# Performance work log

Hardware: AMD Instinct MI355X
Metric: run time of the kernel (lower is better)

## Reference

```python
import jax, jax.numpy as jnp
import numpy as np

D_MODEL, N_STATE, L_MAX, BATCH = 256, 64, 2048, 16

def _to_c(x):
    return jax.lax.complex(x[..., 0], x[..., 1])

def setup_inputs() -> dict:
    key = jax.random.key(0)
    k_u, k_ct_r, k_ct_i, k_step = jax.random.split(key, 4)
    n, d = N_STATE, D_MODEL
    # --- HiPPO DPLR init (numpy, matches torch hippo_dplr) ---
    P = np.sqrt(1.0 + 2.0 * np.arange(1, n + 1, dtype=np.float64))
    A = np.tril(np.outer(P, P)) - np.diag(np.arange(1, n + 1, dtype=np.float64))
    A = -A
    p = 0.5 * np.sqrt(2.0 * np.arange(1, n + 1, dtype=np.float64) + 1.0)
    Ap = (A + np.outer(p, p)).astype(np.complex64)
    lam, V = np.linalg.eig(Ap)
    p_rot = V.conj().T @ p.astype(np.complex64)
    p_ri = np.stack([p_rot.real, p_rot.imag], -1).astype(np.float32)          # (n,2)
    lambda_ri = np.stack([lam.real, lam.imag], -1).astype(np.float32)         # (n,2)
    # --- B init: sqrt(2k+1), repeated over channels, zero imag ---
    B_r = np.sqrt(2.0 * np.arange(1, n + 1) + 1.0).astype(np.float32)
    B_ri = np.stack([np.tile(B_r, (d, 1)), np.zeros((d, n), np.float32)], -1) # (d,n,2)
    # --- Ct: xavier-normal complex ---
    std = float(np.sqrt(2.0 / (d + n)))
    Ct_r = jax.random.normal(k_ct_r, (d, n), jnp.float32) * (std / np.sqrt(2.0))
    Ct_i = jax.random.normal(k_ct_i, (d, n), jnp.float32) * (std / np.sqrt(2.0))
    Ct_ri = jnp.stack([Ct_r, Ct_i], -1)                                        # (d,n,2)
    Dp = jnp.ones((1, 1, d), jnp.float32)
    log_step = jax.random.uniform(k_step, (d,), jnp.float32) * (
        np.log(0.1) - np.log(0.001)) + np.log(0.001)
    u = jax.random.normal(k_u, (BATCH, L_MAX, d), jnp.float32)
    return {"u": u, "p_ri": jnp.asarray(p_ri), "lambda_ri": jnp.asarray(lambda_ri),
            "B_ri": jnp.asarray(B_ri), "Ct_ri": Ct_ri, "Dp": Dp, "log_step": log_step}

def reference(u, p_ri, lambda_ri, B_ri, Ct_ri, Dp, log_step):
    p = _to_c(p_ri)          # (n,)
    lam = _to_c(lambda_ri)   # (n,)
    B = _to_c(B_ri)          # (d,n)
    Ct = _to_c(Ct_ri)        # (d,n)
    L = u.shape[1]
    omega = jnp.exp(2j * jnp.pi * jnp.arange(L) / L).astype(jnp.complex64)  # (L,)
    step = jnp.exp(log_step)                                               # (d,)
    g = (2.0 / step)[:, None] * ((1.0 - omega) / (1.0 + omega))[None, :]   # (d,L)
    c = 2.0 / (1.0 + omega)                                                # (L,)
    inv = 1.0 / (g[:, :, None] - lam[None, None, :])                       # (d,L,n)
    k00 = jnp.einsum('dn,dln->dl', Ct.conj() * B, inv)
    k01 = jnp.einsum('dn,dln->dl', Ct.conj() * p[None, :], inv)
    k10 = jnp.einsum('dn,dln->dl', p.conj()[None, :] * B, inv)
    k11 = jnp.einsum('n,dln->dl', p.conj() * p, inv)
    at_roots = c[None, :] * (k00 - k01 * k10 / (1.0 + k11))                # (d,L)
    out = jnp.fft.ifft(at_roots, n=L, axis=-1)
    order = jnp.concatenate([jnp.zeros((1,), jnp.int32), jnp.arange(L - 1, 0, -1)])
    K = out[:, order].real[None]                                           # (1,d,L)
    # causal FFT convolution
    ud = jnp.fft.rfft(jnp.pad(u, ((0, 0), (0, L), (0, 0))), axis=1)        # (B,L+1,d)
    Kd = jnp.fft.rfft(jnp.pad(K, ((0, 0), (0, 0), (0, L))), axis=-1)       # (1,d,L+1)
    y = jnp.fft.irfft(jnp.transpose(ud, (0, 2, 1)) * Kd, axis=-1)[..., :L]
    y = jnp.transpose(y, (0, 2, 1)).astype(u.dtype)                        # (B,L,d)
    return y + Dp * u
```

## Files before the change

kernel.cpp:

```cpp
#include <hip/hip_runtime.h>
#include <math.h>

#define LLEN   2048
#define NFFT   4096
#define DMODEL 256
#define NSTATE 64
#define NBATCH 16
#define PI_F   3.14159265358979323846f

#define PADIDX(a) ((a) + ((a) >> 4))
#define LDSN  (NFFT + (NFFT >> 4))
#define LDSN2 (LLEN + (LLEN >> 4))
#define KSTRIDE 2056

__device__ inline float frcp(float x) { return __builtin_amdgcn_rcpf(x); }

#define RADIX4(ar0,ai0,ar1,ai1,ar2,ai2,ar3,ai3,S) do {                      \
    float s0r=(ar0)+(ar2), s0i=(ai0)+(ai2);                                 \
    float s1r=(ar0)-(ar2), s1i=(ai0)-(ai2);                                 \
    float s2r=(ar1)+(ar3), s2i=(ai1)+(ai3);                                 \
    float s3r=(ar1)-(ar3), s3i=(ai1)-(ai3);                                 \
    (ar0)=s0r+s2r; (ai0)=s0i+s2i;                                           \
    (ar2)=s0r-s2r; (ai2)=s0i-s2i;                                           \
    (ar1)=s1r-(S)*s3i; (ai1)=s1i+(S)*s3r;                                   \
    (ar3)=s1r+(S)*s3i; (ai3)=s1i-(S)*s3r;                                   \
} while (0)

template<int SIGN>
__device__ inline void dft16(float xr[16], float xi[16]) {
    const float S = (float)SIGN;
    const float C1 = 0.9238795325112867f, S1 = 0.3826834323650898f;
    const float C2 = 0.7071067811865476f;
    RADIX4(xr[0],xi[0], xr[4],xi[4], xr[8],xi[8],  xr[12],xi[12], S);
    RADIX4(xr[1],xi[1], xr[5],xi[5], xr[9],xi[9],  xr[13],xi[13], S);
    RADIX4(xr[2],xi[2], xr[6],xi[6], xr[10],xi[10],xr[14],xi[14], S);
    RADIX4(xr[3],xi[3], xr[7],xi[7], xr[11],xi[11],xr[15],xi[15], S);
#define TW(idx, wr_, wi_) { float tr = xr[idx]*(wr_) - xi[idx]*(wi_);       \
    xi[idx] = xr[idx]*(wi_) + xi[idx]*(wr_); xr[idx] = tr; }
    TW(5,  C1,  S*S1);
    TW(6,  C2,  S*C2);
    TW(7,  S1,  S*C1);
    TW(9,  C2,  S*C2);
    TW(10, 0.f, S);
    TW(11, -C2, S*C2);
    TW(13, S1,  S*C1);
    TW(14, -C2, S*C2);
    TW(15, -C1, -S*S1);
#undef TW
    RADIX4(xr[0],xi[0],  xr[1],xi[1],  xr[2],xi[2],  xr[3],xi[3],  S);
    RADIX4(xr[4],xi[4],  xr[5],xi[5],  xr[6],xi[6],  xr[7],xi[7],  S);
    RADIX4(xr[8],xi[8],  xr[9],xi[9],  xr[10],xi[10],xr[11],xi[11],S);
    RADIX4(xr[12],xi[12],xr[13],xi[13],xr[14],xi[14],xr[15],xi[15],S);
}

template<int SIGN>
__device__ inline void dft8(float xr[8], float xi[8]) {
    const float S = (float)SIGN;
    const float C2 = 0.7071067811865476f;
    RADIX4(xr[0],xi[0], xr[2],xi[2], xr[4],xi[4], xr[6],xi[6], S);
    RADIX4(xr[1],xi[1], xr[3],xi[3], xr[5],xi[5], xr[7],xi[7], S);
    { float tr = xr[3]*C2 - xi[3]*(S*C2); xi[3] = xr[3]*(S*C2) + xi[3]*C2; xr[3] = tr; }
    { float tr = -S*xi[5]; xi[5] = S*xr[5]; xr[5] = tr; }
    { float tr = xr[7]*(-C2) - xi[7]*(S*C2); xi[7] = xr[7]*(S*C2) + xi[7]*(-C2); xr[7] = tr; }
    float br[8], bi[8];
#pragma unroll
    for (int k = 0; k < 4; ++k) {
        br[k]   = xr[2*k] + xr[2*k+1]; bi[k]   = xi[2*k] + xi[2*k+1];
        br[k+4] = xr[2*k] - xr[2*k+1]; bi[k+4] = xi[2*k] - xi[2*k+1];
    }
#pragma unroll
    for (int k = 0; k < 8; ++k) { xr[k] = br[k]; xi[k] = bi[k]; }
}

template<int SIGN>
__device__ inline void tw_apply16(float xr[16], float xi[16], float ang) {
    float wr[16], wi[16];
    __sincosf(ang, &wi[1], &wr[1]);
#pragma unroll
    for (int k = 1; k < 8; ++k) {
        wr[2*k]   = wr[k]*wr[k] - wi[k]*wi[k];
        wi[2*k]   = 2.f * wr[k] * wi[k];
        wr[2*k+1] = wr[k]*wr[k+1] - wi[k]*wi[k+1];
        wi[2*k+1] = wr[k]*wi[k+1] + wi[k]*wr[k+1];
    }
#pragma unroll
    for (int t = 1; t < 16; ++t) {
        float tr = xr[t]*wr[t] - xi[t]*wi[t];
        xi[t] = xr[t]*wi[t] + xi[t]*wr[t];
        xr[t] = tr;
    }
}

template<int SIGN, int M, int L, bool PRUNE>
__device__ inline void stage16(float2* X, int j, bool active) {
    float xr[16], xi[16];
    const int p = j & (L - 1);
    if (active) {
#pragma unroll
        for (int t = 0; t < 16; ++t) {
            float2 v = X[PADIDX(j + t * M)];
            xr[t] = v.x; xi[t] = v.y;
        }
        tw_apply16<SIGN>(xr, xi, ((float)SIGN * 2.f * PI_F / (float)(16 * L)) * (float)p);
        dft16<SIGN>(xr, xi);
    }
    __syncthreads();
    if (active) {
        const int base = 16 * j - 15 * p;
#pragma unroll
        for (int k0 = 0; k0 < 4; ++k0)
#pragma unroll
            for (int k2 = 0; k2 < 4; ++k2) {
                const int u = k0 + 4 * k2;
                if (!PRUNE || u < 8) {
                    const int a = base + u * L;
                    X[PADIDX(a)] = make_float2(xr[4*k0+k2], xi[4*k0+k2]);
                }
            }
    }
    __syncthreads();
}

template<int SIGN, bool ZHI, bool PRUNE>
__device__ inline void fft4096_f2(float2* X, int tid) {
    float xr[16], xi[16];
#pragma unroll
    for (int t = 0; t < 16; ++t) {
        if (ZHI && t >= 8) { xr[t] = 0.f; xi[t] = 0.f; }
        else { float2 v = X[PADIDX(tid + t * 256)]; xr[t] = v.x; xi[t] = v.y; }
    }
    dft16<SIGN>(xr, xi);
    __syncthreads();
#pragma unroll
    for (int k0 = 0; k0 < 4; ++k0)
#pragma unroll
        for (int k2 = 0; k2 < 4; ++k2)
            X[PADIDX(16 * tid + k0 + 4 * k2)] = make_float2(xr[4*k0+k2], xi[4*k0+k2]);
    __syncthreads();
    stage16<SIGN, 256, 16,  false>(X, tid, true);
    stage16<SIGN, 256, 256, PRUNE>(X, tid, true);
}

template<int SIGN>
__device__ inline void fft2048_f2(float2* X, int tid) {
    float xr[8], xi[8];
#pragma unroll
    for (int t = 0; t < 8; ++t) {
        float2 v = X[PADIDX(tid + t * 256)];
        xr[t] = v.x; xi[t] = v.y;
    }
    dft8<SIGN>(xr, xi);
    __syncthreads();
#pragma unroll
    for (int u = 0; u < 8; ++u)
        X[PADIDX(8 * tid + u)] = make_float2(xr[u], xi[u]);
    __syncthreads();
    stage16<SIGN, 128, 8,   false>(X, tid, tid < 128);
    stage16<SIGN, 128, 128, false>(X, tid, tid < 128);
}

__global__ __launch_bounds__(256) void k_ar(const float* __restrict__ p_ri,
                                            const float* __restrict__ lambda_ri,
                                            const float* __restrict__ B_ri,
                                            const float* __restrict__ Ct_ri,
                                            const float* __restrict__ log_step,
                                            float2* __restrict__ ar_out) {
    __shared__ float4 c0[NSTATE], c1[NSTATE];
    __shared__ float2 lam[NSTATE];
    const int d = blockIdx.x >> 3;
    const int l = ((blockIdx.x & 7) << 8) | threadIdx.x;
    const int tid = threadIdx.x;
    if (tid < NSTATE) {
        const int n = tid;
        const float px = p_ri[2*n], py = p_ri[2*n+1];
        lam[n] = make_float2(lambda_ri[2*n], lambda_ri[2*n+1]);
        const float Bx = B_ri[(d*NSTATE+n)*2], By = B_ri[(d*NSTATE+n)*2+1];
        const float Cx = Ct_ri[(d*NSTATE+n)*2], Cy = Ct_ri[(d*NSTATE+n)*2+1];
        c0[n] = make_float4(Cx*Bx + Cy*By, Cx*By - Cy*Bx,
                            Cx*px + Cy*py, Cx*py - Cy*px);
        c1[n] = make_float4(px*Bx + py*By, px*By - py*Bx, px*px + py*py, 0.f);
    }
    __syncthreads();

    const float tos = 2.f * __expf(-log_step[d]);
    float sn, cs;
    sincosf(2.f * PI_F * (float)l / (float)LLEN, &sn, &cs);
    const float opx = 1.f + cs, opy = sn;
    const float omx = 1.f - cs, omy = -sn;
    const float inv_op = frcp(opx*opx + opy*opy);
    const float gx = tos * (omx*opx + omy*opy) * inv_op;
    const float gy = tos * (omy*opx - omx*opy) * inv_op;
    const float ccx = 2.f * opx * inv_op, ccy = -2.f * opy * inv_op;

    float k00x = 0, k00y = 0, k01x = 0, k01y = 0;
    float k10x = 0, k10y = 0, k11x = 0, k11y = 0;
    for (int n = 0; n < NSTATE; ++n) {
        const float2 lm = lam[n];
        const float dx = gx - lm.x, dy = gy - lm.y;
        const float idn = frcp(dx*dx + dy*dy);
        const float ix = dx * idn, iy = -dy * idn;
        const float4 a = c0[n];
        const float4 b = c1[n];
        k00x += a.x*ix - a.y*iy;  k00y += a.x*iy + a.y*ix;
        k01x += a.z*ix - a.w*iy;  k01y += a.z*iy + a.w*ix;
        k10x += b.x*ix - b.y*iy;  k10y += b.x*iy + b.y*ix;
        k11x += b.z*ix;           k11y += b.z*iy;
    }
    const float nx = k01x*k10x - k01y*k10y;
    const float ny = k01x*k10y + k01y*k10x;
    const float dpx = 1.f + k11x, dpy = k11y;
    const float idq = frcp(dpx*dpx + dpy*dpy);
    const float qx = (nx*dpx + ny*dpy) * idq;
    const float qy = (ny*dpx - nx*dpy) * idq;
    const float rx = k00x - qx, ry = k00y - qy;
    ar_out[(size_t)d * LLEN + l] = make_float2(ccx*rx - ccy*ry, ccx*ry + ccy*rx);
}

__global__ __launch_bounds__(256, 4) void k_mix(const float* __restrict__ u,
                                                const float2* __restrict__ a_in,
                                                float* __restrict__ ut,
                                                float2* __restrict__ Hc) {
    __shared__ float2 X[LDSN2];
    const int tid = threadIdx.x;

    if (blockIdx.x >= DMODEL) {
        const int blk = blockIdx.x - DMODEL;
        const int bt0 = (blk & 1023) * 32;
        const int ch0 = (blk >> 10) * 32;
        float* tile = (float*)X;
        const int tx = tid & 31, ty = tid >> 5;
#pragma unroll
        for (int k = 0; k < 4; ++k) {
            const int r = ty + 8 * k;
            tile[r * 33 + tx] = u[(size_t)(bt0 + r) * DMODEL + ch0 + tx];
        }
        __syncthreads();
#pragma unroll
        for (int k = 0; k < 4; ++k) {
            const int r = ty + 8 * k;
            ut[(size_t)(ch0 + r) * (NBATCH * LLEN) + bt0 + tx] = tile[tx * 33 + r];
        }
        return;
    }

    const int d = blockIdx.x;
    const float isc = 1.f / (float)NFFT;
    const float4* a4 = (const float4*)(a_in + (size_t)d * LLEN);
#pragma unroll
    for (int k = 0; k < 4; ++k) {
        const int v = tid + k * 256;
        const float4 w = a4[v];
        X[PADIDX(2 * v)]     = make_float2(w.x, w.y);
        X[PADIDX(2 * v + 1)] = make_float2(w.z, w.w);
    }
    __syncthreads();

    float2* H = Hc + (size_t)d * KSTRIDE;
    for (int m = tid; m <= 1024; m += 256) {
        const float2 am = X[PADIDX(m)];
        const float2 an = X[PADIDX((LLEN - m) & (LLEN - 1))];
        H[2 * m] = make_float2((an.x + am.x) * 0.5f * isc,
                               (an.y - am.y) * 0.5f * isc);
    }
    fft2048_f2<-1>(X, tid);

#pragma unroll
    for (int k = 0; k < 8; ++k) {
        const int j = tid + k * 256;
        const int q = PADIDX(j);
        const float Kj = X[q].x * (1.f / (float)LLEN);
        float snj, csj;
        __sincosf(-PI_F * (float)j * (1.f / 2048.f), &snj, &csj);
        X[q] = make_float2(Kj * csj, Kj * snj);
    }
    __syncthreads();
    fft2048_f2<-1>(X, tid);

    for (int m = tid; m < 1024; m += 256) {
        const float2 w = X[PADIDX(m)];
        H[2 * m + 1] = make_float2(w.x * isc, w.y * isc);
    }
}

__global__ __launch_bounds__(256, 4) void k_conv(const float* __restrict__ ut,
                                                 const float2* __restrict__ Hc,
                                                 float* __restrict__ yt) {
    __shared__ float2 X[LDSN];
    const int ch = blockIdx.x >> 3, pair = blockIdx.x & 7, tid = threadIdx.x;
    const float4* u0 = (const float4*)(ut + (size_t)ch * (NBATCH * LLEN) + (size_t)(2 * pair) * LLEN);
    const float4* u1 = u0 + LLEN / 4;
#pragma unroll
    for (int k = 0; k < 2; ++k) {
        const int v4 = tid + k * 256;
        const float4 a = u0[v4], b = u1[v4];
        const int base = 4 * v4;
        X[PADIDX(base + 0)] = make_float2(a.x, b.x);
        X[PADIDX(base + 1)] = make_float2(a.y, b.y);
        X[PADIDX(base + 2)] = make_float2(a.z, b.z);
        X[PADIDX(base + 3)] = make_float2(a.w, b.w);
    }
    __syncthreads();
    fft4096_f2<-1, true, false>(X, tid);

    const float2* H = Hc + (size_t)ch * KSTRIDE;
    for (int f = tid; f <= NFFT / 2; f += 256) {
        const int fb = (NFFT - f) & (NFFT - 1);
        const float2 Za = X[PADIDX(f)], Zb = X[PADIDX(fb)];
        const float u0x = 0.5f * (Za.x + Zb.x), u0y = 0.5f * (Za.y - Zb.y);
        const float u1x = 0.5f * (Za.y + Zb.y), u1y = -0.5f * (Za.x - Zb.x);
        const float2 Ha = H[f];
        const float y0x = u0x*Ha.x - u0y*Ha.y, y0y = u0x*Ha.y + u0y*Ha.x;
        const float y1x = u1x*Ha.x - u1y*Ha.y, y1y = u1x*Ha.y + u1y*Ha.x;
        X[PADIDX(f)] = make_float2(y0x - y1y, y0y + y1x);
        if (fb != f) {
            const float Hbx = Ha.x, Hby = -Ha.y;
            const float z0x = u0x*Hbx + u0y*Hby, z0y = u0x*Hby - u0y*Hbx;
            const float z1x = u1x*Hbx + u1y*Hby, z1y = u1x*Hby - u1y*Hbx;
            X[PADIDX(fb)] = make_float2(z0x - z1y, z0y + z1x);
        }
    }
    __syncthreads();
    fft4096_f2<+1, false, true>(X, tid);

    float* y0o = yt + (size_t)ch * (NBATCH * LLEN) + (size_t)(2 * pair) * LLEN;
    float* y1o = y0o + LLEN;
    for (int i = tid; i < LLEN; i += 256) {
        const float2 v = X[PADIDX(i)];
        y0o[i] = v.x;
        y1o[i] = v.y;
    }
}

__global__ __launch_bounds__(256) void k_post(const float* __restrict__ yt,
                                              const float* __restrict__ u,
                                              const float* __restrict__ Dp,
                                              float* __restrict__ out) {
    __shared__ float tile[32][33];
    const int bt0 = blockIdx.x * 32, ch0 = blockIdx.y * 32;
    const int tid = threadIdx.x;
    {
        const int r = tid >> 3, c = (tid & 7) * 4;
        const float4 v = *(const float4*)&yt[(size_t)(ch0 + r) * (NBATCH * LLEN) + bt0 + c];
        tile[r][c] = v.x; tile[r][c+1] = v.y; tile[r][c+2] = v.z; tile[r][c+3] = v.w;
    }
    __syncthreads();
    {
        const int r = tid >> 3, c4 = (tid & 7) * 4;
        const size_t idx = (size_t)(bt0 + r) * DMODEL + ch0 + c4;
        const float4 uv = *(const float4*)&u[idx];
        const float4 dp = *(const float4*)&Dp[ch0 + c4];
        float4 o;
        o.x = tile[c4 + 0][r] + dp.x * uv.x;
        o.y = tile[c4 + 1][r] + dp.y * uv.y;
        o.z = tile[c4 + 2][r] + dp.z * uv.z;
        o.w = tile[c4 + 3][r] + dp.w * uv.w;
        *(float4*)&out[idx] = o;
    }
}

extern "C" void kernel_launch(void* const* d_in, const int* in_sizes, int n_in,
                              void* d_out, int out_size, void* d_ws, size_t ws_size,
                              hipStream_t stream) {
    const float* u         = (const float*)d_in[0];
    const float* p_ri      = (const float*)d_in[1];
    const float* lambda_ri = (const float*)d_in[2];
    const float* B_ri      = (const float*)d_in[3];
    const float* Ct_ri     = (const float*)d_in[4];
    const float* Dp        = (const float*)d_in[5];
    const float* log_step  = (const float*)d_in[6];
    float* out = (float*)d_out;

    float2* Hc = (float2*)d_ws;
    char*   wb = (char*)d_ws + (size_t)DMODEL * KSTRIDE * sizeof(float2);
    float2* a  = (float2*)wb;
    float*  yt = (float*)wb;
    float*  ut = out;

    k_ar  <<<DMODEL * 8, 256, 0, stream>>>(p_ri, lambda_ri, B_ri, Ct_ri, log_step, a);
    k_mix <<<DMODEL + 8192, 256, 0, stream>>>(u, a, ut, Hc);
    k_conv<<<DMODEL * (NBATCH / 2), 256, 0, stream>>>(ut, Hc, yt);
    k_post<<<dim3(NBATCH * LLEN / 32, DMODEL / 32), 256, 0, stream>>>(yt, u, Dp, out);
}
```

Measured before the change: 176.8 us.

## Fuse transpose, convolution and skip-add into one kernel pairing adjacent channels

Drops the separate transpose of u and the post-transpose/skip kernel. The convolution kernel now reads u directly with strided float2 loads, covering two adjacent channels of one batch packed as real and imaginary parts. It multiplies each by its own channel filter and writes the output with the D*u term added in place. This removes two full global round-trips through the ut/yt intermediates and one launch, at the cost of strided, partially coalesced loads and stores (8 bytes per row of 1 KB).

Measured after the change: 179.4 us. No clear change (+1.5%).

```diff
diff --git a/kernel.cpp b/kernel.cpp
--- a/kernel.cpp
+++ b/kernel.cpp
@@ -216,33 +216,10 @@
     ar_out[(size_t)d * LLEN + l] = make_float2(ccx*rx - ccy*ry, ccx*ry + ccy*rx);
 }
 
-__global__ __launch_bounds__(256, 4) void k_mix(const float* __restrict__ u,
-                                                const float2* __restrict__ a_in,
-                                                float* __restrict__ ut,
+__global__ __launch_bounds__(256, 4) void k_mix(const float2* __restrict__ a_in,
                                                 float2* __restrict__ Hc) {
     __shared__ float2 X[LDSN2];
     const int tid = threadIdx.x;
-
-    if (blockIdx.x >= DMODEL) {
-        const int blk = blockIdx.x - DMODEL;
-        const int bt0 = (blk & 1023) * 32;
-        const int ch0 = (blk >> 10) * 32;
-        float* tile = (float*)X;
-        const int tx = tid & 31, ty = tid >> 5;
-#pragma unroll
-        for (int k = 0; k < 4; ++k) {
-            const int r = ty + 8 * k;
-            tile[r * 33 + tx] = u[(size_t)(bt0 + r) * DMODEL + ch0 + tx];
-        }
-        __syncthreads();
-#pragma unroll
-        for (int k = 0; k < 4; ++k) {
-            const int r = ty + 8 * k;
-            ut[(size_t)(ch0 + r) * (NBATCH * LLEN) + bt0 + tx] = tile[tx * 33 + r];
-        }
-        return;
-    }
-
     const int d = blockIdx.x;
     const float isc = 1.f / (float)NFFT;
     const float4* a4 = (const float4*)(a_in + (size_t)d * LLEN);
@@ -282,79 +259,55 @@
     }
 }
 
-__global__ __launch_bounds__(256, 4) void k_conv(const float* __restrict__ ut,
-                                                 const float2* __restrict__ Hc,
-                                                 float* __restrict__ yt) {
+__global__ __launch_bounds__(256, 4) void k_fused(const float* __restrict__ u,
+                                                  const float2* __restrict__ Hc,
+                                                  const float* __restrict__ Dp,
+                                                  float* __restrict__ out) {
     __shared__ float2 X[LDSN];
-    const int ch = blockIdx.x >> 3, pair = blockIdx.x & 7, tid = threadIdx.x;
-    const float4* u0 = (const float4*)(ut + (size_t)ch * (NBATCH * LLEN) + (size_t)(2 * pair) * LLEN);
-    const float4* u1 = u0 + LLEN / 4;
-#pragma unroll
-    for (int k = 0; k < 2; ++k) {
-        const int v4 = tid + k * 256;
-        const float4 a = u0[v4], b = u1[v4];
-        const int base = 4 * v4;
-        X[PADIDX(base + 0)] = make_float2(a.x, b.x);
-        X[PADIDX(base + 1)] = make_float2(a.y, b.y);
-        X[PADIDX(base + 2)] = make_float2(a.z, b.z);
-        X[PADIDX(base + 3)] = make_float2(a.w, b.w);
+    const int i = blockIdx.x;
+    const int x = i & 7;
+    const int s = i >> 3;
+    const int b  = s >> 4;
+    const int cp = (x << 4) | (s & 15);
+    const int ch = cp * 2;
+    const int tid = threadIdx.x;
+
+    const float* ub = u + (size_t)b * (LLEN * DMODEL) + ch;
+    float2 uv[8];
+#pragma unroll
+    for (int k = 0; k < 8; ++k) {
+        const int t = tid + k * 256;
+        uv[k] = *(const float2*)(ub + (size_t)t * DMODEL);
+        X[PADIDX(t)] = uv[k];
     }
     __syncthreads();
     fft4096_f2<-1, true, false>(X, tid);
 
-    const float2* H = Hc + (size_t)ch * KSTRIDE;
+    const float2* Ha = Hc + (size_t)ch * KSTRIDE;
+    const float2* Hb = Ha + KSTRIDE;
     for (int f = tid; f <= NFFT / 2; f += 256) {
         const int fb = (NFFT - f) & (NFFT - 1);
         const float2 Za = X[PADIDX(f)], Zb = X[PADIDX(fb)];
-        const float u0x = 0.5f * (Za.x + Zb.x), u0y = 0.5f * (Za.y - Zb.y);
-        const float u1x = 0.5f * (Za.y + Zb.y), u1y = -0.5f * (Za.x - Zb.x);
-        const float2 Ha = H[f];
-        const float y0x = u0x*Ha.x - u0y*Ha.y, y0y = u0x*Ha.y + u0y*Ha.x;
-        const float y1x = u1x*Ha.x - u1y*Ha.y, y1y = u1x*Ha.y + u1y*Ha.x;
-        X[PADIDX(f)] = make_float2(y0x - y1y, y0y + y1x);
-        if (fb != f) {
-            const float Hbx = Ha.x, Hby = -Ha.y;
-            const float z0x = u0x*Hbx + u0y*Hby, z0y = u0x*Hby - u0y*Hbx;
-            const float z1x = u1x*Hbx + u1y*Hby, z1y = u1x*Hby - u1y*Hbx;
-            X[PADIDX(fb)] = make_float2(z0x - z1y, z0y + z1x);
-        }
+        const float xax = 0.5f * (Za.x + Zb.x), xay = 0.5f * (Za.y - Zb.y);
+        const float xbx = 0.5f * (Za.y + Zb.y), xby = -0.5f * (Za.x - Zb.x);
+        const float2 A = Ha[f], B = Hb[f];
+        const float yax = xax*A.x - xay*A.y, yay = xax*A.y + xay*A.x;
+        const float ybx = xbx*B.x - xby*B.y, yby = xbx*B.y + xby*B.x;
+        X[PADIDX(f)] = make_float2(yax - yby, yay + ybx);
+        if (fb != f)
+            X[PADIDX(fb)] = make_float2(yax + yby, ybx - yay);
     }
     __syncthreads();
     fft4096_f2<+1, false, true>(X, tid);
 
-    float* y0o = yt + (size_t)ch * (NBATCH * LLEN) + (size_t)(2 * pair) * LLEN;
-    float* y1o = y0o + LLEN;
-    for (int i = tid; i < LLEN; i += 256) {
-        const float2 v = X[PADIDX(i)];
-        y0o[i] = v.x;
-        y1o[i] = v.y;
-    }
-}
-
-__global__ __launch_bounds__(256) void k_post(const float* __restrict__ yt,
-                                              const float* __restrict__ u,
-                                              const float* __restrict__ Dp,
-                                              float* __restrict__ out) {
-    __shared__ float tile[32][33];
-    const int bt0 = blockIdx.x * 32, ch0 = blockIdx.y * 32;
-    const int tid = threadIdx.x;
-    {
-        const int r = tid >> 3, c = (tid & 7) * 4;
-        const float4 v = *(const float4*)&yt[(size_t)(ch0 + r) * (NBATCH * LLEN) + bt0 + c];
-        tile[r][c] = v.x; tile[r][c+1] = v.y; tile[r][c+2] = v.z; tile[r][c+3] = v.w;
-    }
-    __syncthreads();
-    {
-        const int r = tid >> 3, c4 = (tid & 7) * 4;
-        const size_t idx = (size_t)(bt0 + r) * DMODEL + ch0 + c4;
-        const float4 uv = *(const float4*)&u[idx];
-        const float4 dp = *(const float4*)&Dp[ch0 + c4];
-        float4 o;
-        o.x = tile[c4 + 0][r] + dp.x * uv.x;
-        o.y = tile[c4 + 1][r] + dp.y * uv.y;
-        o.z = tile[c4 + 2][r] + dp.z * uv.z;
-        o.w = tile[c4 + 3][r] + dp.w * uv.w;
-        *(float4*)&out[idx] = o;
+    const float2 dp = *(const float2*)(Dp + ch);
+    float* ob = out + (size_t)b * (LLEN * DMODEL) + ch;
+#pragma unroll
+    for (int k = 0; k < 8; ++k) {
+        const int t = tid + k * 256;
+        const float2 v = X[PADIDX(t)];
+        *(float2*)(ob + (size_t)t * DMODEL) =
+            make_float2(v.x + dp.x * uv[k].x, v.y + dp.y * uv[k].y);
     }
 }
 
@@ -371,13 +324,9 @@
     float* out = (float*)d_out;
 
     float2* Hc = (float2*)d_ws;
-    char*   wb = (char*)d_ws + (size_t)DMODEL * KSTRIDE * sizeof(float2);
-    float2* a  = (float2*)wb;
-    float*  yt = (float*)wb;
-    float*  ut = out;
-
-    k_ar  <<<DMODEL * 8, 256, 0, stream>>>(p_ri, lambda_ri, B_ri, Ct_ri, log_step, a);
-    k_mix <<<DMODEL + 8192, 256, 0, stream>>>(u, a, ut, Hc);
-    k_conv<<<DMODEL * (NBATCH / 2), 256, 0, stream>>>(ut, Hc, yt);
-    k_post<<<dim3(NBATCH * LLEN / 32, DMODEL / 32), 256, 0, stream>>>(yt, u, Dp, out);
-}
+    float2* a  = (float2*)((char*)d_ws + (size_t)DMODEL * KSTRIDE * sizeof(float2));
+
+    k_ar   <<<DMODEL * 8, 256, 0, stream>>>(p_ri, lambda_ri, B_ri, Ct_ri, log_step, a);
+    k_mix  <<<DMODEL, 256, 0, stream>>>(a, Hc);
+    k_fused<<<NBATCH * (DMODEL / 2), 256, 0, stream>>>(u, Hc, Dp, out);
+}
```
